# Kernel tuning notes

Hardware: AMD Instinct MI355X
Metric: run time of the kernel (lower is better)

The kernel has to match this reference:

```python
import jax, jax.numpy as jnp
import numpy as np

H, D = 8, 16
HID = H * D  # hidden_channels = 128
SQRT_D = float(np.sqrt(D))


def setup_inputs() -> dict:
    key = jax.random.key(0)
    ks = iter(jax.random.split(key, 64))
    def nrm(shape, scale):
        return jax.random.normal(next(ks), shape, dtype=jnp.float32) * scale
    def rint(n, hi):
        return jax.random.randint(next(ks), (n,), 0, hi, dtype=jnp.int32)
    E = 250000
    Nh, Ni, Nt = 8000, 40000, 20000
    inp = {
        'x_herb': nrm((Nh, 400), 1.0),
        'x_ing':  nrm((Ni, 300), 1.0),
        'x_tgt':  nrm((Nt, 200), 1.0),
        # per-type input projections
        'W_herb': nrm((400, HID), 0.05), 'b_herb': jnp.zeros((HID,), jnp.float32),
        'W_ing':  nrm((300, HID), 0.06), 'b_ing':  jnp.zeros((HID,), jnp.float32),
        'W_tgt':  nrm((200, HID), 0.07), 'b_tgt':  jnp.zeros((HID,), jnp.float32),
        # HGTConv per-node-type k/q/v linears, stacked over [herb, ing, tgt]
        'Wk': nrm((3, HID, HID), 0.09), 'bk': jnp.zeros((3, HID), jnp.float32),
        'Wq': nrm((3, HID, HID), 0.09), 'bq': jnp.zeros((3, HID), jnp.float32),
        'Wv': nrm((3, HID, HID), 0.09), 'bv': jnp.zeros((3, HID), jnp.float32),
        # per-edge-type relation matrices / priors, stacked over 4 edge types
        'a_rel': nrm((4, H, D, D), 0.25),
        'm_rel': nrm((4, H, D, D), 0.25),
        'p_rel': jnp.ones((4, H), jnp.float32),
        # per-dst-node-type output linear + skip gate
        'Wa': nrm((3, HID, HID), 0.09), 'ba': jnp.zeros((3, HID), jnp.float32),
        'skip': jnp.ones((3,), jnp.float32),
        # final herb linear
        'W_out': nrm((HID, HID), 0.09), 'b_out': jnp.zeros((HID,), jnp.float32),
        # edge lists: (herb->ing contains), (ing->herb rev), (ing->tgt targets), (tgt->ing rev)
        'src_ci': rint(E, Nh), 'dst_ci': rint(E, Ni),
        'src_ic': rint(E, Ni), 'dst_ic': rint(E, Nh),
        'src_it': rint(E, Ni), 'dst_it': rint(E, Nt),
        'src_ti': rint(E, Nt), 'dst_ti': rint(E, Ni),
    }
    return inp


def _hetero_forward(x_herb, x_ing, x_tgt, W_herb, b_herb, W_ing, b_ing, W_tgt, b_tgt,
                    Wk, bk, Wq, bq, Wv, bv, a_rel, m_rel, p_rel, Wa, ba, skip,
                    W_out, b_out, src_ci, dst_ci, src_ic, dst_ic, src_it, dst_it,
                    src_ti, dst_ti):
    types = ['herb', 'ing', 'tgt']
    xs = {'herb': x_herb @ W_herb + b_herb,
          'ing':  x_ing  @ W_ing  + b_ing,
          'tgt':  x_tgt  @ W_tgt  + b_tgt}
    Ns = {t: xs[t].shape[0] for t in types}
    # per-node-type k/q/v, reshaped to [N, H, D]
    k = {t: (xs[t] @ Wk[i] + bk[i]).reshape(-1, H, D) for i, t in enumerate(types)}
    q = {t: (xs[t] @ Wq[i] + bq[i]).reshape(-1, H, D) for i, t in enumerate(types)}
    v = {t: (xs[t] @ Wv[i] + bv[i]).reshape(-1, H, D) for i, t in enumerate(types)}

    edge_defs = [  # (edge_type_id, src_type, dst_type, src_idx, dst_idx)
        (0, 'herb', 'ing', src_ci, dst_ci),
        (1, 'ing', 'herb', src_ic, dst_ic),
        (2, 'ing', 'tgt', src_it, dst_it),
        (3, 'tgt', 'ing', src_ti, dst_ti),
    ]
    contrib = {t: [] for t in types}
    for e, s, t, src, dst in edge_defs:
        # relation-specific transforms at node level, then gather per edge
        k_rel = jnp.einsum('nhd,hde->nhe', k[s], a_rel[e])  # [Ns, H, D]
        v_rel = jnp.einsum('nhd,hde->nhe', v[s], m_rel[e])  # [Ns, H, D]
        logit = (q[t][dst] * k_rel[src]).sum(-1) * (p_rel[e] / SQRT_D)  # [E, H]
        contrib[t].append((logit, v_rel[src], dst))

    out = {}
    for i, t in enumerate(types):
        logits = jnp.concatenate([c[0] for c in contrib[t]], axis=0)  # [Et, H]
        msgs = jnp.concatenate([c[1] for c in contrib[t]], axis=0)    # [Et, H, D]
        dsts = jnp.concatenate([c[2] for c in contrib[t]], axis=0)    # [Et]
        n = Ns[t]
        # segment softmax over all incoming edges of each dst node (per head)
        mx = jax.ops.segment_max(logits, dsts, num_segments=n)
        ex = jnp.exp(logits - mx[dsts])
        den = jax.ops.segment_sum(ex, dsts, num_segments=n)
        alpha = ex / (den[dsts] + 1e-16)
        agg = jax.ops.segment_sum(msgs * alpha[:, :, None], dsts, num_segments=n)
        agg = agg.reshape(n, HID)
        o = jax.nn.gelu(agg, approximate=False) @ Wa[i] + ba[i]
        g = jax.nn.sigmoid(skip[i])
        out[t] = jax.nn.relu(g * o + (1.0 - g) * xs[t])
    out_herb = out['herb'] @ W_out + b_out
    return (out_herb, out['ing'], out['tgt'])


def reference(x_herb, x_ing, x_tgt, W_herb, b_herb, W_ing, b_ing, W_tgt, b_tgt,
              Wk, bk, Wq, bq, Wv, bv, a_rel, m_rel, p_rel, Wa, ba, skip,
              W_out, b_out, src_ci, dst_ci, src_ic, dst_ic, src_it, dst_it,
              src_ti, dst_ti):
    return _hetero_forward(x_herb, x_ing, x_tgt, W_herb, b_herb, W_ing, b_ing,
                           W_tgt, b_tgt, Wk, bk, Wq, bq, Wv, bv, a_rel, m_rel,
                           p_rel, Wa, ba, skip, W_out, b_out, src_ci, dst_ci,
                           src_ic, dst_ic, src_it, dst_it, src_ti, dst_ti)
```

## Files before the change

kernel.cpp:

```cpp
#include <hip/hip_runtime.h>
#include <math.h>

#define HID 128
typedef unsigned int uint;
typedef unsigned short ushort;
typedef __attribute__((ext_vector_type(8))) short short8;
typedef __attribute__((ext_vector_type(4))) float floatx4;
typedef __attribute__((ext_vector_type(2))) float f32x2;

__device__ __forceinline__ ushort f2b(float f) {
  uint u = __float_as_uint(f);
  u += 0x7fffu + ((u >> 16) & 1u);
  return (ushort)(u >> 16);
}
__device__ __forceinline__ float b2f(ushort s) {
  return __uint_as_float(((uint)s) << 16);
}
__device__ __forceinline__ float blo(uint u) { return __uint_as_float(u << 16); }
__device__ __forceinline__ float bhi(uint u) { return __uint_as_float(u & 0xffff0000u); }
__device__ __forceinline__ f32x2 b2x2(uint u) {
  f32x2 r;
  r.x = __uint_as_float(u << 16);
  r.y = __uint_as_float(u & 0xffff0000u);
  return r;
}

__device__ __forceinline__ void gll16(const ushort* g, ushort* l) {
  __builtin_amdgcn_global_load_lds(
      (const __attribute__((address_space(1))) void*)g,
      (__attribute__((address_space(3))) void*)l, 16, 0, 0);
}

__device__ __forceinline__ size_t a_packed_us(int rr, int col) {
  int tm = rr >> 7, prow = rr & 127;
  int ptk = col >> 5, kin = col & 31;
  int sw = (kin >> 3) ^ ((prow >> 1) & 3);
  return (((size_t)tm * 4 + ptk) * 512 + (size_t)prow * 4 + sw) * 8 + (kin & 7);
}

#define CSR_CH 2048
#define CSR_SH 9

struct EdgeStreams {
  const int* src[4]; const int* dst[4];
  int off[4]; uint rel[4]; uint ldb[4];
};

struct PackSeg { const float* X; ushort* out; int M, K, Ktiles, start; };
struct WBlk { const float* src; ushort* dst; int K; int start; };
struct Prolog {
  PackSeg pk[3];
  int crwstart, wstart, bstart, total;
  const float *Wk, *bk, *Wv, *bv, *a_rel, *m_rel, *p_rel;
  ushort* kw_dst[4];
  ushort* vw_dst[4];
  float* bcat;
  int kb_off[4], vb_off[4];
  WBlk wb[10];
  const float* bq;
  int bq_off[3];
  const int* edst[4];
  int eoff[4];
  uint* hist;
  int NBs, NBH, NBK, E;
};

__device__ void combine_rel_elem(const Prolog& P, int idx)
{
  int col  = idx & 127;
  int rest = idx >> 7;
  int row  = rest % 129;
  rest /= 129;
  int kv = rest & 1;
  int e  = rest >> 1;
  int i  = (e + 1) >> 1;
  int h = col >> 4, j = col & 15;
  const float* Wsrc = kv ? P.Wv : P.Wk;
  const float* bsrc = kv ? P.bv : P.bk;
  const float* rel  = kv ? P.m_rel : P.a_rel;
  float acc = 0.f;
  if (row < 128) {
#pragma unroll
    for (int d = 0; d < 16; ++d)
      acc += Wsrc[(size_t)i * 16384 + (size_t)row * 128 + h * 16 + d] *
             rel[((e * 8 + h) * 16 + d) * 16 + j];
  } else {
#pragma unroll
    for (int d = 0; d < 16; ++d)
      acc += bsrc[i * 128 + h * 16 + d] * rel[((e * 8 + h) * 16 + d) * 16 + j];
  }
  if (!kv) acc *= P.p_rel[e * 8 + h] * 0.36067376022224085f;
  if (row < 128) {
    ushort* dst = kv ? P.vw_dst[e] : P.kw_dst[e];
    int tk = row >> 5, chunk = (row >> 3) & 3, m = row & 7;
    int swf = chunk ^ ((col >> 1) & 3);
    dst[((tk * 512 + col * 4 + swf) << 3) + m] = f2b(acc);
  } else {
    P.bcat[(kv ? P.vb_off[e] : P.kb_off[e]) + col] = acc;
  }
}

__device__ void conv_elem(const Prolog& P, int s0)
{
  int si = 0;
#pragma unroll
  for (int k = 1; k < 10; ++k)
    if (s0 >= P.wb[k].start) si = k;
  WBlk b = P.wb[si];
  int s = s0 - b.start;
  int tk = s >> 9, o = s & 511;
  int c = o >> 2, swf = o & 3;
  int chunk = swf ^ ((c >> 1) & 3);
  int r0 = tk * 32 + chunk * 8;
  ushort tmp[8];
#pragma unroll
  for (int m = 0; m < 8; ++m) {
    int r = r0 + m;
    tmp[m] = (r < b.K) ? f2b(b.src[(size_t)r * 128 + c]) : (ushort)0;
  }
  *(short8*)&b.dst[(size_t)s * 8] = *(short8*)tmp;
}

__global__ __launch_bounds__(256)
void prologue(Prolog P)
{
  __shared__ uint h[512];
  int bI = blockIdx.x;
  if (bI < P.NBH) {
    int et = bI / P.NBs;
    int i0 = (bI - et * P.NBs) * CSR_CH;
    const int* dp = P.edst[et];
    int off = P.eoff[et];
    for (int t = threadIdx.x; t < P.NBK; t += 256) h[t] = 0;
    __syncthreads();
#pragma unroll
    for (int j = 0; j < CSR_CH / 256; ++j) {
      int idx = i0 + j * 256 + threadIdx.x;
      if (idx < P.E) atomicAdd(&h[(uint)(off + dp[idx]) >> CSR_SH], 1u);
    }
    __syncthreads();
    for (int t = threadIdx.x; t < P.NBK; t += 256)
      P.hist[(size_t)t * P.NBH + bI] = h[t];
    return;
  }
  int gtid = (bI - P.NBH) * 256 + threadIdx.x;
  if (gtid >= P.total) return;
  if (gtid >= P.bstart) {
    int j = gtid - P.bstart;
    P.bcat[P.bq_off[j >> 7] + (j & 127)] = P.bq[j];
    return;
  }
  if (gtid >= P.wstart) { conv_elem(P, gtid - P.wstart); return; }
  if (gtid >= P.crwstart) { combine_rel_elem(P, gtid - P.crwstart); return; }
  int si = 0;
  if (gtid >= P.pk[2].start) si = 2;
  else if (gtid >= P.pk[1].start) si = 1;
  const PackSeg s = P.pk[si];
  int slot = gtid - s.start;
  int spm = s.Ktiles << 9;
  int tm = slot / spm, r2 = slot - tm * spm;
  int tk = r2 >> 9, o = r2 & 511;
  int row = o >> 2, sw = o & 3;
  int chunk = sw ^ ((row >> 1) & 3);
  int grow = tm * 128 + row;
  int gk = tk * 32 + chunk * 8;
  ushort tmp[8];
  if (grow < s.M && gk + 8 <= s.K) {
    const float* p = s.X + (size_t)grow * s.K + gk;
    float4 a = *(const float4*)p, b = *(const float4*)(p + 4);
    tmp[0] = f2b(a.x); tmp[1] = f2b(a.y); tmp[2] = f2b(a.z); tmp[3] = f2b(a.w);
    tmp[4] = f2b(b.x); tmp[5] = f2b(b.y); tmp[6] = f2b(b.z); tmp[7] = f2b(b.w);
  } else {
#pragma unroll
    for (int j = 0; j < 8; ++j) {
      int kk = gk + j;
      tmp[j] = (grow < s.M && kk < s.K) ? f2b(s.X[(size_t)grow * s.K + kk]) : (ushort)0;
    }
  }
  *(short8*)&s.out[(size_t)slot * 8] = *(short8*)tmp;
}

__global__ __launch_bounds__(256)
void bucket_scan(uint* __restrict__ hist, uint* __restrict__ bucketTot, int NBH)
{
  __shared__ uint ws[4];
  __shared__ uint carry_s;
  int b = blockIdx.x;
  int t = threadIdx.x, lane = t & 63, w = t >> 6;
  if (t == 0) carry_s = 0;
  __syncthreads();
  for (int base = 0; base < NBH; base += 256) {
    int i = base + t;
    uint x = (i < NBH) ? hist[(size_t)b * NBH + i] : 0u;
    uint v = x;
#pragma unroll
    for (int o = 1; o < 64; o <<= 1) {
      uint y = __shfl_up(v, o, 64);
      if (lane >= o) v += y;
    }
    if (lane == 63) ws[w] = v;
    __syncthreads();
    uint add = carry_s;
    for (int k = 0; k < w; ++k) add += ws[k];
    if (i < NBH) hist[(size_t)b * NBH + i] = add + v - x;
    __syncthreads();
    if (t == 255) carry_s = add + v;
    __syncthreads();
  }
  if (t == 0) bucketTot[b] = carry_s;
}

__device__ __forceinline__ void base_scan(const uint* __restrict__ bucketTot,
                                          uint* sb, uint* ws, int NBK)
{
  int t = threadIdx.x, lane = t & 63, w = t >> 6;
  sb[t] = (t < NBK) ? bucketTot[t] : 0u;
  sb[t + 256] = (t + 256 < NBK) ? bucketTot[t + 256] : 0u;
  __syncthreads();
  uint a0 = sb[2 * t], a1 = sb[2 * t + 1];
  uint s = a0 + a1;
  uint v = s;
#pragma unroll
  for (int o = 1; o < 64; o <<= 1) {
    uint y = __shfl_up(v, o, 64);
    if (lane >= o) v += y;
  }
  if (lane == 63) ws[w] = v;
  __syncthreads();
  uint add = 0;
  for (int k = 0; k < w; ++k) add += ws[k];
  uint e0 = add + v - s;
  sb[2 * t] = e0;
  sb[2 * t + 1] = e0 + a0;
  __syncthreads();
}

__global__ __launch_bounds__(256)
void bucket_scatter(EdgeStreams es, const uint* __restrict__ hist,
                    const uint* __restrict__ bucketTot,
                    uint2* __restrict__ inter, int NBs, int NBH, int NBK, int E)
{
  __shared__ uint sb[516];
  __shared__ uint ws[4];
  __shared__ uint cur[512];
  base_scan(bucketTot, sb, ws, NBK);
  int b = blockIdx.x;
  int et = b / NBs;
  int i0 = (b - et * NBs) * CSR_CH;
  const int* dp = es.dst[et];
  const int* sp = es.src[et];
  int off = es.off[et];
  uint rel = es.rel[et], ldb = es.ldb[et];
  for (int t = threadIdx.x; t < NBK; t += 256)
    cur[t] = sb[t] + hist[(size_t)t * NBH + b];
  __syncthreads();
#pragma unroll
  for (int j = 0; j < CSR_CH / 256; ++j) {
    int idx = i0 + j * 256 + threadIdx.x;
    if (idx < E) {
      int g = off + dp[idx];
      uint pos = atomicAdd(&cur[(uint)g >> CSR_SH], 1u);
      inter[pos] = make_uint2(rel + (uint)sp[idx] * ldb, (uint)g);
    }
  }
}

__global__ __launch_bounds__(256)
void bucket_finalize(const uint2* __restrict__ inter,
                     const uint* __restrict__ bucketTot,
                     int* __restrict__ starts, uint* __restrict__ payload,
                     int Ntot, int NBK)
{
  __shared__ uint sb[516];
  __shared__ uint ncnt[512];
  __shared__ uint ws[4];
  base_scan(bucketTot, sb, ws, NBK);
  int b = blockIdx.x;
  int g0 = b << CSR_SH;
  int t = threadIdx.x, lane = t & 63, w = t >> 6;
  uint r0 = sb[b], r1 = sb[b + 1];
  if (b == NBK - 1 && t == 0) starts[Ntot] = (int)r1;
  ncnt[t] = 0; ncnt[t + 256] = 0;
  __syncthreads();
  for (uint i = r0 + t; i < r1; i += 256)
    atomicAdd(&ncnt[inter[i].y - g0], 1u);
  __syncthreads();
  uint a0 = ncnt[2 * t], a1 = ncnt[2 * t + 1];
  uint s = a0 + a1;
  uint v = s;
#pragma unroll
  for (int o = 1; o < 64; o <<= 1) {
    uint y = __shfl_up(v, o, 64);
    if (lane >= o) v += y;
  }
  if (lane == 63) ws[w] = v;
  __syncthreads();
  uint add = r0;
  for (int k = 0; k < w; ++k) add += ws[k];
  uint e0 = add + v - s;
  int gi = g0 + 2 * t;
  if (gi < Ntot)     starts[gi]     = (int)e0;
  if (gi + 1 < Ntot) starts[gi + 1] = (int)(e0 + a0);
  ncnt[2 * t] = e0;
  ncnt[2 * t + 1] = e0 + a0;
  __syncthreads();
  for (uint i = r0 + t; i < r1; i += 256) {
    uint2 rec = inter[i];
    uint pos = atomicAdd(&ncnt[rec.y - g0], 1u);
    payload[pos] = rec.x;
  }
}

struct GemmSeg {
  const ushort* A; const ushort* B; const float* bias;
  void* out; const ushort* xsP;
  int Ktiles, ldo, Mreal, skip_idx, epi, NT, start;
  int n2; const ushort* B2; const float* bias2;
  void* out2; int ldo2, Mreal2, epi2;
};
struct Gemm3 { GemmSeg s[3]; const float* skip; int nseg; };

__launch_bounds__(256)
__global__ void gemm_sched(Gemm3 g3)
{
  __shared__ __align__(16) ushort lds[20480];
  ushort* Xs = lds + 12288;

  int bid = blockIdx.x;
  int si = 0;
  if (g3.nseg > 1 && bid >= g3.s[1].start)
    si = (g3.nseg > 2 && bid >= g3.s[2].start) ? 2 : 1;
  const GemmSeg sg = g3.s[si];
  int local = bid - sg.start;
  int tmH = local / sg.NT, tn = local - tmH * sg.NT;
  int tm = tmH >> 1, hm = tmH & 1;

  const int t = threadIdx.x;
  const int wave = t >> 6, lane = t & 63;
  const int wn = wave * 32;
  const int l16 = lane & 15, quad = lane >> 4;
  const int Ktiles = sg.Ktiles;
  const int swz = (quad ^ ((l16 >> 1) & 3)) * 8;

  const ushort* Ahalf = sg.A + ((size_t)tm * Ktiles) * 4096 + hm * 2048;
  const ushort* Bbase = sg.B + (size_t)tn * Ktiles * 4096;

  floatx4 acc[4][2];
#pragma unroll
  for (int i = 0; i < 4; ++i)
#pragma unroll
    for (int j = 0; j < 2; ++j) acc[i][j] = (floatx4){0.f, 0.f, 0.f, 0.f};

  auto stage = [&](int tk, int buf) {
#pragma unroll
    for (int j = 0; j < 3; ++j) {
      int c = wave * 3 + j;
      if (c < 4)
        gll16(Ahalf + (size_t)tk * 4096 + c * 512 + lane * 8,
              lds + buf * 2048 + c * 512);
      else
        gll16(Bbase + (size_t)tk * 4096 + (c - 4) * 512 + lane * 8,
              lds + 4096 + buf * 4096 + (c - 4) * 512);
    }
  };
  auto stage2L = [&](int s2, int buf) {
#pragma unroll
    for (int j = 0; j < 2; ++j) {
      int c = wave * 2 + j;
      gll16(sg.B2 + (size_t)s2 * 4096 + c * 512 + lane * 8,
            lds + buf * 4096 + c * 512);
    }
  };

  stage(0, 0);
  __syncthreads();

  for (int tk = 0; tk < Ktiles; ++tk) {
    int buf = tk & 1;
    if (tk + 1 < Ktiles) stage(tk + 1, buf ^ 1);

    short8 af[4], bfr[2];
#pragma unroll
    for (int i = 0; i < 4; ++i)
      af[i] = *(const short8*)&lds[buf * 2048 + (i * 16 + l16) * 32 + swz];
#pragma unroll
    for (int n = 0; n < 2; ++n)
      bfr[n] = *(const short8*)&lds[4096 + buf * 4096 + (wn + n * 16 + l16) * 32 + swz];
#pragma unroll
    for (int mi = 0; mi < 4; ++mi)
#pragma unroll
      for (int ni = 0; ni < 2; ++ni)
        acc[mi][ni] = __builtin_amdgcn_mfma_f32_16x16x32_bf16(
            bfr[ni], af[mi], acc[mi][ni], 0, 0, 0);
    __syncthreads();
  }

  if (sg.n2 > 0) stage2L(0, 0);

  const int epi = sg.epi;
  float g = 0.f, omg = 0.f;
  if (epi == 2 || epi == 3 || epi == 5) {
    float s = g3.skip[sg.skip_idx];
    g = 1.f / (1.f + __expf(-s));
    omg = 1.f - g;
  }
#pragma unroll
  for (int ni = 0; ni < 2; ++ni) {
    int cl = wn + ni * 16 + quad * 4;
    int cb = tn * 128 + cl;
    float4 b4 = *(const float4*)&sg.bias[cb];
#pragma unroll
    for (int mi = 0; mi < 4; ++mi) {
      int prow = mi * 16 + l16;
      int rr = tm * 128 + hm * 64 + prow;
      float v0 = acc[mi][ni][0] + b4.x;
      float v1 = acc[mi][ni][1] + b4.y;
      float v2 = acc[mi][ni][2] + b4.z;
      float v3 = acc[mi][ni][3] + b4.w;
      if (epi == 0) {
        uint2 o = make_uint2(((uint)f2b(v1) << 16) | f2b(v0),
                             ((uint)f2b(v3) << 16) | f2b(v2));
        *(uint2*)&((ushort*)sg.out)[(size_t)rr * sg.ldo + cb] = o;
      } else if (epi == 1) {
        if (rr < sg.Mreal)
          *(float4*)&((float*)sg.out)[(size_t)rr * sg.ldo + cb] =
              make_float4(v0, v1, v2, v3);
      } else if (epi == 2) {
        if (rr < sg.Mreal) {
          uint2 xo = *(const uint2*)&sg.xsP[a_packed_us(rr, cb)];
          float4 o;
          o.x = fmaxf(g * v0 + omg * blo(xo.x), 0.f);
          o.y = fmaxf(g * v1 + omg * bhi(xo.x), 0.f);
          o.z = fmaxf(g * v2 + omg * blo(xo.y), 0.f);
          o.w = fmaxf(g * v3 + omg * bhi(xo.y), 0.f);
          *(float4*)&((float*)sg.out)[(size_t)rr * sg.ldo + cb] = o;
        }
      } else if (epi == 3) {
        uint2 xo = *(const uint2*)&sg.xsP[a_packed_us(rr, cb)];
        uint2 o = make_uint2(
            ((uint)f2b(fmaxf(g * v1 + omg * bhi(xo.x), 0.f)) << 16) |
                   f2b(fmaxf(g * v0 + omg * blo(xo.x), 0.f)),
            ((uint)f2b(fmaxf(g * v3 + omg * bhi(xo.y), 0.f)) << 16) |
                   f2b(fmaxf(g * v2 + omg * blo(xo.y), 0.f)));
        *(uint2*)&((ushort*)sg.out)[a_packed_us(rr, cb)] = o;
      } else if (epi == 4) {
        uint2 o = make_uint2(((uint)f2b(v1) << 16) | f2b(v0),
                             ((uint)f2b(v3) << 16) | f2b(v2));
        *(uint2*)&((ushort*)sg.out)[a_packed_us(rr, cb)] = o;
        int kin = cl & 31;
        int sw2 = (kin >> 3) ^ ((prow >> 1) & 3);
        *(uint2*)&Xs[(cl >> 5) * 2048 + prow * 32 + sw2 * 8 + (kin & 7)] = o;
      } else {
        uint2 xo = *(const uint2*)&sg.xsP[a_packed_us(rr, cb)];
        uint2 o = make_uint2(
            ((uint)f2b(fmaxf(g * v1 + omg * bhi(xo.x), 0.f)) << 16) |
                   f2b(fmaxf(g * v0 + omg * blo(xo.x), 0.f)),
            ((uint)f2b(fmaxf(g * v3 + omg * bhi(xo.y), 0.f)) << 16) |
                   f2b(fmaxf(g * v2 + omg * blo(xo.y), 0.f)));
        int kin = cl & 31;
        int sw2 = (kin >> 3) ^ ((prow >> 1) & 3);
        *(uint2*)&Xs[(cl >> 5) * 2048 + prow * 32 + sw2 * 8 + (kin & 7)] = o;
      }
    }
  }

  if (sg.n2 == 0) return;
  __syncthreads();
  int total2 = sg.n2 * 4;
  floatx4 a2[4][2];
#pragma unroll
  for (int i = 0; i < 4; ++i)
#pragma unroll
    for (int j = 0; j < 2; ++j) a2[i][j] = (floatx4){0.f, 0.f, 0.f, 0.f};
  for (int s2 = 0; s2 < total2; ++s2) {
    int buf = s2 & 1;
    if (s2 + 1 < total2) stage2L(s2 + 1, buf ^ 1);
    int xb = (s2 & 3) * 2048;
    short8 af[4], bfr[2];
#pragma unroll
    for (int i = 0; i < 4; ++i)
      af[i] = *(const short8*)&Xs[xb + (i * 16 + l16) * 32 + swz];
#pragma unroll
    for (int n = 0; n < 2; ++n)
      bfr[n] = *(const short8*)&lds[buf * 4096 + (wn + n * 16 + l16) * 32 + swz];
#pragma unroll
    for (int mi = 0; mi < 4; ++mi)
#pragma unroll
      for (int ni = 0; ni < 2; ++ni)
        a2[mi][ni] = __builtin_amdgcn_mfma_f32_16x16x32_bf16(
            bfr[ni], af[mi], a2[mi][ni], 0, 0, 0);
    __syncthreads();
    if ((s2 & 3) == 3) {
      int t2 = s2 >> 2;
#pragma unroll
      for (int ni = 0; ni < 2; ++ni) {
        int cb2 = t2 * 128 + wn + ni * 16 + quad * 4;
        float4 b4 = *(const float4*)&sg.bias2[cb2];
#pragma unroll
        for (int mi = 0; mi < 4; ++mi) {
          int rr = tm * 128 + hm * 64 + mi * 16 + l16;
          float v0 = a2[mi][ni][0] + b4.x;
          float v1 = a2[mi][ni][1] + b4.y;
          float v2 = a2[mi][ni][2] + b4.z;
          float v3 = a2[mi][ni][3] + b4.w;
          if (sg.epi2 == 0) {
            uint2 o = make_uint2(((uint)f2b(v1) << 16) | f2b(v0),
                                 ((uint)f2b(v3) << 16) | f2b(v2));
            *(uint2*)&((ushort*)sg.out2)[(size_t)rr * sg.ldo2 + cb2] = o;
          } else {
            if (rr < sg.Mreal2)
              *(float4*)&((float*)sg.out2)[(size_t)rr * sg.ldo2 + cb2] =
                  make_float4(v0, v1, v2, v3);
          }
          a2[mi][ni] = (floatx4){0.f, 0.f, 0.f, 0.f};
        }
      }
    }
  }
}

struct GatherType { const ushort* q; ushort* agg; int ldq; };
struct GatherDesc { GatherType ty[3]; int n0, n1; };

__launch_bounds__(256)
__global__ void gather_all(const int* __restrict__ starts,
                           const uint* __restrict__ payload,
                           const ushort* __restrict__ kvbase,
                           GatherDesc gd, int Ntot)
{
  int wid = (blockIdx.x * 256 + threadIdx.x) >> 6;
  if (wid >= Ntot) return;
  int lane = threadIdx.x & 63;
  int g = lane >> 4, l = lane & 15;

  GatherType T;
  int d;
  if (wid < gd.n0)      { T = gd.ty[0]; d = wid; }
  else if (wid < gd.n1) { T = gd.ty[1]; d = wid - gd.n0; }
  else                  { T = gd.ty[2]; d = wid - gd.n1; }

  const char* kvb = (const char*)kvbase;
  const uint lofs = (uint)l * 16u;

  uint4 qv = *(const uint4*)(T.q + (size_t)d * T.ldq + l * 8);
  f32x2 q0 = b2x2(qv.x), q1 = b2x2(qv.y), q2 = b2x2(qv.z), q3 = b2x2(qv.w);

  int e0 = starts[wid], e1 = starts[wid + 1];
  float lsum = 0.f;
  f32x2 ac0 = {0.f, 0.f}, ac1 = {0.f, 0.f}, ac2 = {0.f, 0.f}, ac3 = {0.f, 0.f};

  for (int eb = e0; eb < e1; eb += 8) {
    int eA = eb + g, eB = eA + 4;
    bool actA = eA < e1, actB = eB < e1;
    uint pA = payload[actA ? eA : e0];
    uint pB = payload[actB ? eB : e0];
    const char* bA = kvb + (pA + lofs);
    const char* bB = kvb + (pB + lofs);
    uint4 kA = *(const uint4*)bA;
    uint4 vA = *(const uint4*)(bA + 256);
    uint4 kB = *(const uint4*)bB;
    uint4 vB = *(const uint4*)(bB + 256);

    f32x2 dA = q0 * b2x2(kA.x);
    dA = __builtin_elementwise_fma(q1, b2x2(kA.y), dA);
    dA = __builtin_elementwise_fma(q2, b2x2(kA.z), dA);
    dA = __builtin_elementwise_fma(q3, b2x2(kA.w), dA);
    f32x2 dB = q0 * b2x2(kB.x);
    dB = __builtin_elementwise_fma(q1, b2x2(kB.y), dB);
    dB = __builtin_elementwise_fma(q2, b2x2(kB.z), dB);
    dB = __builtin_elementwise_fma(q3, b2x2(kB.w), dB);
    float pa = dA.x + dA.y;
    float pb = dB.x + dB.y;
    pa += __shfl_xor(pa, 1, 64);
    pb += __shfl_xor(pb, 1, 64);
    float exA = exp2f(fminf(pa, 115.4f));
    float exB = exp2f(fminf(pb, 115.4f));
    exA = actA ? exA : 0.f;
    exB = actB ? exB : 0.f;
    lsum += exA + exB;
    f32x2 xA = {exA, exA}, xB = {exB, exB};
    ac0 = __builtin_elementwise_fma(xA, b2x2(vA.x), ac0);
    ac1 = __builtin_elementwise_fma(xA, b2x2(vA.y), ac1);
    ac2 = __builtin_elementwise_fma(xA, b2x2(vA.z), ac2);
    ac3 = __builtin_elementwise_fma(xA, b2x2(vA.w), ac3);
    ac0 = __builtin_elementwise_fma(xB, b2x2(vB.x), ac0);
    ac1 = __builtin_elementwise_fma(xB, b2x2(vB.y), ac1);
    ac2 = __builtin_elementwise_fma(xB, b2x2(vB.z), ac2);
    ac3 = __builtin_elementwise_fma(xB, b2x2(vB.w), ac3);
  }

  float s0 = ac0.x, s1 = ac0.y, s2 = ac1.x, s3 = ac1.y;
  float s4 = ac2.x, s5 = ac2.y, s6 = ac3.x, s7 = ac3.y;
#define MRG(v) v += __shfl_xor(v, 16, 64); v += __shfl_xor(v, 32, 64)
  MRG(lsum); MRG(s0); MRG(s1); MRG(s2); MRG(s3); MRG(s4); MRG(s5); MRG(s6); MRG(s7);
#undef MRG

  float inv = 1.f / (lsum + 1e-16f);
  float m0 = (g & 1) ? s2 : s0, m1 = (g & 1) ? s6 : s4;
  float n0 = (g & 1) ? s3 : s1, n1 = (g & 1) ? s7 : s5;
  float x0 = ((g & 2) ? m1 : m0) * inv;
  float x1 = ((g & 2) ? n1 : n0) * inv;
  float g0 = 0.5f * x0 * (1.f + erff(x0 * 0.70710678118654752f));
  float g1 = 0.5f * x1 * (1.f + erff(x1 * 0.70710678118654752f));
  int tm = d >> 7, row = d & 127;
  int tk = l >> 2, sw = (l & 3) ^ ((row >> 1) & 3);
  size_t us = (((size_t)tm * 4 + tk) * 512 + (size_t)row * 4 + sw) * 8 + 2 * g;
  *(uint*)(T.agg + us) = ((uint)f2b(g1) << 16) | (uint)f2b(g0);
}

extern "C" void kernel_launch(void* const* d_in, const int* in_sizes, int n_in,
                              void* d_out, int out_size, void* d_ws, size_t ws_size,
                              hipStream_t stream)
{
  const float* x_herb = (const float*)d_in[0];
  const float* x_ing  = (const float*)d_in[1];
  const float* x_tgt  = (const float*)d_in[2];
  const float* W_herb = (const float*)d_in[3];
  const float* b_herb = (const float*)d_in[4];
  const float* W_ing  = (const float*)d_in[5];
  const float* b_ing  = (const float*)d_in[6];
  const float* W_tgt  = (const float*)d_in[7];
  const float* b_tgt  = (const float*)d_in[8];
  const float* Wk     = (const float*)d_in[9];
  const float* bk     = (const float*)d_in[10];
  const float* Wq     = (const float*)d_in[11];
  const float* bq     = (const float*)d_in[12];
  const float* Wv     = (const float*)d_in[13];
  const float* bv     = (const float*)d_in[14];
  const float* a_rel  = (const float*)d_in[15];
  const float* m_rel  = (const float*)d_in[16];
  const float* p_rel  = (const float*)d_in[17];
  const float* Wa     = (const float*)d_in[18];
  const float* ba     = (const float*)d_in[19];
  const float* skip   = (const float*)d_in[20];
  const float* W_out  = (const float*)d_in[21];
  const float* b_out  = (const float*)d_in[22];
  const int* srcs[4] = {(const int*)d_in[23], (const int*)d_in[25],
                        (const int*)d_in[27], (const int*)d_in[29]};
  const int* dsts[4] = {(const int*)d_in[24], (const int*)d_in[26],
                        (const int*)d_in[28], (const int*)d_in[30]};

  const int Nh = in_sizes[0] / 400;
  const int Ni = in_sizes[1] / 300;
  const int Nt = in_sizes[2] / 200;
  const int E  = in_sizes[23];
  const int Ntot = Nh + Ni + Nt;

  const int MT_h = (Nh + 127) / 128, MT_i = (Ni + 127) / 128, MT_t = (Nt + 127) / 128;
  const int KT_h = 13, KT_i = 10, KT_t = 7;

  const int NBs = (E + CSR_CH - 1) / CSR_CH;
  const int NBH = 4 * NBs;
  const int NBK = (Ntot + (1 << CSR_SH) - 1) >> CSR_SH;

  char* base = (char*)d_ws;
  size_t off = 0;
  auto A = [&](size_t bytes) -> void* {
    void* p = base + off; off += (bytes + 255) & ~(size_t)255; return p;
  };
  ushort* xp_h  = (ushort*)A((size_t)MT_h * KT_h * 8192);
  ushort* xp_i  = (ushort*)A((size_t)MT_i * KT_i * 8192);
  ushort* xp_t  = (ushort*)A((size_t)MT_t * KT_t * 8192);
  ushort* xsP_h = (ushort*)A((size_t)MT_h * 4 * 8192);
  ushort* xsP_i = (ushort*)A((size_t)MT_i * 4 * 8192);
  ushort* xsP_t = (ushort*)A((size_t)MT_t * 4 * 8192);
  ushort* fused_h = (ushort*)A((size_t)MT_h * 128 * 384 * 2);
  ushort* fused_i = (ushort*)A((size_t)MT_i * 128 * 640 * 2);
  ushort* fused_t = (ushort*)A((size_t)MT_t * 128 * 384 * 2);
  ushort* aggp_h  = (ushort*)A((size_t)MT_h * 4 * 8192);
  ushort* aggp_i  = (ushort*)A((size_t)MT_i * 4 * 8192);
  ushort* aggp_t  = (ushort*)A((size_t)MT_t * 4 * 8192);
  ushort* Weff1_h = (ushort*)A((size_t)KT_h * 8192);
  ushort* Weff1_i = (ushort*)A((size_t)KT_i * 8192);
  ushort* Weff1_t = (ushort*)A((size_t)KT_t * 8192);
  ushort* Wcat_h = (ushort*)A((size_t)3 * 4 * 8192);
  ushort* Wcat_i = (ushort*)A((size_t)5 * 4 * 8192);
  ushort* Wcat_t = (ushort*)A((size_t)3 * 4 * 8192);
  float* bcat   = (float*)A(1408 * 4);
  ushort* Wa_t   = (ushort*)A((size_t)3 * 16384 * 2);
  ushort* Wout_t = (ushort*)A((size_t)16384 * 2);
  int* starts  = (int*)A((size_t)(Ntot + 4) * 4);
  uint* payload = (uint*)A((size_t)(4 * E + 8) * 4);
  uint* hist    = (uint*)A((size_t)NBK * NBH * 4);
  uint* bucketTot  = (uint*)A((size_t)NBK * 4);
  uint2* inter  = (uint2*)A((size_t)(4 * E + 8) * 8);
  (void)ws_size; (void)n_in;

  const int toff_h = 0, toff_i = Nh, toff_t = Nh + Ni;
  dim3 blk(256);

  uint fi2 = (uint)((size_t)(fused_i - fused_h) * 2);
  uint ft2 = (uint)((size_t)(fused_t - fused_h) * 2);

  int sl_h = MT_h * KT_h * 512, sl_i = MT_i * KT_i * 512, sl_t = MT_t * KT_t * 512;
  Prolog P;
  P.pk[0] = {x_herb, xp_h, Nh, 400, KT_h, 0};
  P.pk[1] = {x_ing,  xp_i, Ni, 300, KT_i, sl_h};
  P.pk[2] = {x_tgt,  xp_t, Nt, 200, KT_t, sl_h + sl_i};
  P.crwstart = sl_h + sl_i + sl_t;
  P.wstart = P.crwstart + 4 * 2 * 129 * 128;
  {
    const float* wsrc10[10] = {W_herb, W_ing, W_tgt, Wq, Wq + 16384, Wq + 32768,
                               Wa, Wa + 16384, Wa + 32768, W_out};
    ushort* wdst10[10] = {Weff1_h, Weff1_i, Weff1_t, Wcat_h, Wcat_i, Wcat_t,
                          Wa_t, Wa_t + 16384, Wa_t + 32768, Wout_t};
    int wk10[10] = {400, 300, 200, 128, 128, 128, 128, 128, 128, 128};
    int wcum = 0;
    for (int z = 0; z < 10; ++z) {
      P.wb[z] = {wsrc10[z], wdst10[z], wk10[z], wcum};
      wcum += ((wk10[z] + 31) / 32) * 512;
    }
    P.bstart = P.wstart + wcum;
  }
  P.total = P.bstart + 384;
  P.Wk = Wk; P.bk = bk; P.Wv = Wv; P.bv = bv;
  P.a_rel = a_rel; P.m_rel = m_rel; P.p_rel = p_rel;
  P.kw_dst[0] = Wcat_h + 16384; P.vw_dst[0] = Wcat_h + 32768;
  P.kw_dst[1] = Wcat_i + 16384; P.vw_dst[1] = Wcat_i + 32768;
  P.kw_dst[2] = Wcat_i + 49152; P.vw_dst[2] = Wcat_i + 65536;
  P.kw_dst[3] = Wcat_t + 16384; P.vw_dst[3] = Wcat_t + 32768;
  P.bcat = bcat;
  P.kb_off[0] = 128;  P.vb_off[0] = 256;
  P.kb_off[1] = 512;  P.vb_off[1] = 640;
  P.kb_off[2] = 768;  P.vb_off[2] = 896;
  P.kb_off[3] = 1152; P.vb_off[3] = 1280;
  P.bq = bq;
  P.bq_off[0] = 0; P.bq_off[1] = 384; P.bq_off[2] = 1024;
  P.edst[0] = dsts[0]; P.eoff[0] = toff_i;
  P.edst[1] = dsts[1]; P.eoff[1] = toff_h;
  P.edst[2] = dsts[2]; P.eoff[2] = toff_t;
  P.edst[3] = dsts[3]; P.eoff[3] = toff_i;
  P.hist = hist; P.NBs = NBs; P.NBH = NBH; P.NBK = NBK; P.E = E;
  prologue<<<NBH + (P.total + 255) / 256, blk, 0, stream>>>(P);

  EdgeStreams ES;
  ES.src[0] = srcs[0]; ES.dst[0] = dsts[0]; ES.off[0] = toff_i;
  ES.rel[0] = 256u;        ES.ldb[0] = 768u;
  ES.src[1] = srcs[1]; ES.dst[1] = dsts[1]; ES.off[1] = toff_h;
  ES.rel[1] = fi2 + 256u;  ES.ldb[1] = 1280u;
  ES.src[2] = srcs[2]; ES.dst[2] = dsts[2]; ES.off[2] = toff_t;
  ES.rel[2] = fi2 + 768u;  ES.ldb[2] = 1280u;
  ES.src[3] = srcs[3]; ES.dst[3] = dsts[3]; ES.off[3] = toff_i;
  ES.rel[3] = ft2 + 256u;  ES.ldb[3] = 768u;
  bucket_scan<<<NBK, blk, 0, stream>>>(hist, bucketTot, NBH);
  bucket_scatter<<<NBH, blk, 0, stream>>>(ES, hist, bucketTot, inter, NBs, NBH, NBK, E);
  bucket_finalize<<<NBK, blk, 0, stream>>>(inter, bucketTot, starts, payload, Ntot, NBK);

  Gemm3 G1;
  G1.skip = skip; G1.nseg = 3;
  G1.s[0] = {xp_h, Weff1_h, b_herb, xsP_h, nullptr, KT_h, 0, 0, 0, 4, 1, 0,
             3, Wcat_h, bcat + 0, fused_h, 384, 0, 0};
  G1.s[1] = {xp_i, Weff1_i, b_ing,  xsP_i, nullptr, KT_i, 0, 0, 0, 4, 1, 2 * MT_h,
             5, Wcat_i, bcat + 384, fused_i, 640, 0, 0};
  G1.s[2] = {xp_t, Weff1_t, b_tgt,  xsP_t, nullptr, KT_t, 0, 0, 0, 4, 1,
             2 * (MT_h + MT_i),
             3, Wcat_t, bcat + 1024, fused_t, 384, 0, 0};
  gemm_sched<<<2 * (MT_h + MT_i + MT_t), blk, 0, stream>>>(G1);

  GatherDesc GD;
  GD.n0 = Nh; GD.n1 = Nh + Ni;
  GD.ty[0] = {fused_h, aggp_h, 384};
  GD.ty[1] = {fused_i, aggp_i, 640};
  GD.ty[2] = {fused_t, aggp_t, 384};
  gather_all<<<(Ntot + 3) / 4, blk, 0, stream>>>(starts, payload, fused_h, GD, Ntot);

  float* outp = (float*)d_out;
  float* out_herb = outp;
  float* out_ing  = outp + (size_t)Nh * HID;
  float* out_tgt  = outp + (size_t)(Nh + Ni) * HID;
  Gemm3 GE;
  GE.skip = skip; GE.nseg = 3;
  GE.s[0] = {aggp_h, Wa_t + 0 * 16384, ba + 0 * 128, nullptr, xsP_h,
             4, 0, 0, 0, 5, 1, 0,
             1, Wout_t, b_out, out_herb, 128, Nh, 1};
  GE.s[1] = {aggp_i, Wa_t + 1 * 16384, ba + 1 * 128, out_ing, xsP_i,
             4, 128, Ni, 1, 2, 1, 2 * MT_h,
             0, nullptr, nullptr, nullptr, 0, 0, 0};
  GE.s[2] = {aggp_t, Wa_t + 2 * 16384, ba + 2 * 128, out_tgt, xsP_t,
             4, 128, Nt, 2, 2, 1, 2 * (MT_h + MT_i),
             0, nullptr, nullptr, nullptr, 0, 0, 0};
  gemm_sched<<<2 * (MT_h + MT_i + MT_t), blk, 0, stream>>>(GE);
  (void)out_size;
}
```

Measured before the change: 378.9 us.

## Fuse fp32-to-bf16 input packing into first GEMM A-tile staging

Removes the prologue stage that converted x_herb/x_ing/x_tgt to swizzled bf16 tiles in a global scratch buffer. The first GEMM now loads fp32 rows directly, converts them to bf16 in registers and writes them into the swizzled LDS layout. The B operand keeps its async global-to-LDS load. This drops one full write and read of the packed inputs and shrinks the prologue, at the cost of synchronous fp32 loads and conversions in the GEMM's staging path, which may reduce overlap with the MFMA work.

```diff
diff --git a/kernel.cpp b/kernel.cpp
--- a/kernel.cpp
+++ b/kernel.cpp
@@ -46,11 +46,9 @@
   int off[4]; uint rel[4]; uint ldb[4];
 };
 
-struct PackSeg { const float* X; ushort* out; int M, K, Ktiles, start; };
 struct WBlk { const float* src; ushort* dst; int K; int start; };
 struct Prolog {
-  PackSeg pk[3];
-  int crwstart, wstart, bstart, total;
+  int wstart, bstart, total;
   const float *Wk, *bk, *Wv, *bv, *a_rel, *m_rel, *p_rel;
   ushort* kw_dst[4];
   ushort* vw_dst[4];
@@ -151,33 +149,7 @@
     return;
   }
   if (gtid >= P.wstart) { conv_elem(P, gtid - P.wstart); return; }
-  if (gtid >= P.crwstart) { combine_rel_elem(P, gtid - P.crwstart); return; }
-  int si = 0;
-  if (gtid >= P.pk[2].start) si = 2;
-  else if (gtid >= P.pk[1].start) si = 1;
-  const PackSeg s = P.pk[si];
-  int slot = gtid - s.start;
-  int spm = s.Ktiles << 9;
-  int tm = slot / spm, r2 = slot - tm * spm;
-  int tk = r2 >> 9, o = r2 & 511;
-  int row = o >> 2, sw = o & 3;
-  int chunk = sw ^ ((row >> 1) & 3);
-  int grow = tm * 128 + row;
-  int gk = tk * 32 + chunk * 8;
-  ushort tmp[8];
-  if (grow < s.M && gk + 8 <= s.K) {
-    const float* p = s.X + (size_t)grow * s.K + gk;
-    float4 a = *(const float4*)p, b = *(const float4*)(p + 4);
-    tmp[0] = f2b(a.x); tmp[1] = f2b(a.y); tmp[2] = f2b(a.z); tmp[3] = f2b(a.w);
-    tmp[4] = f2b(b.x); tmp[5] = f2b(b.y); tmp[6] = f2b(b.z); tmp[7] = f2b(b.w);
-  } else {
-#pragma unroll
-    for (int j = 0; j < 8; ++j) {
-      int kk = gk + j;
-      tmp[j] = (grow < s.M && kk < s.K) ? f2b(s.X[(size_t)grow * s.K + kk]) : (ushort)0;
-    }
-  }
-  *(short8*)&s.out[(size_t)slot * 8] = *(short8*)tmp;
+  combine_rel_elem(P, gtid);
 }
 
 __global__ __launch_bounds__(256)
@@ -317,6 +289,7 @@
   int Ktiles, ldo, Mreal, skip_idx, epi, NT, start;
   int n2; const ushort* B2; const float* bias2;
   void* out2; int ldo2, Mreal2, epi2;
+  const float* Af; int Kf, Mf;
 };
 struct Gemm3 { GemmSeg s[3]; const float* skip; int nseg; };
 
@@ -345,22 +318,46 @@
   const ushort* Ahalf = sg.A + ((size_t)tm * Ktiles) * 4096 + hm * 2048;
   const ushort* Bbase = sg.B + (size_t)tn * Ktiles * 4096;
 
+  const int aprow = t >> 2, asw = t & 3;
+  const int achunk = asw ^ ((aprow >> 1) & 3);
+  const int agrow = tm * 128 + hm * 64 + aprow;
+  const bool arowok = (sg.Af == nullptr) || (agrow < sg.Mf);
+  const float* axrow = sg.Af + (size_t)(arowok ? agrow : 0) * sg.Kf;
+
   floatx4 acc[4][2];
 #pragma unroll
   for (int i = 0; i < 4; ++i)
 #pragma unroll
     for (int j = 0; j < 2; ++j) acc[i][j] = (floatx4){0.f, 0.f, 0.f, 0.f};
 
-  auto stage = [&](int tk, int buf) {
-#pragma unroll
-    for (int j = 0; j < 3; ++j) {
-      int c = wave * 3 + j;
-      if (c < 4)
-        gll16(Ahalf + (size_t)tk * 4096 + c * 512 + lane * 8,
-              lds + buf * 2048 + c * 512);
-      else
-        gll16(Bbase + (size_t)tk * 4096 + (c - 4) * 512 + lane * 8,
-              lds + 4096 + buf * 4096 + (c - 4) * 512);
+  auto stageA = [&](int tk, int buf) {
+    if (sg.Af == nullptr) {
+      gll16(Ahalf + (size_t)tk * 4096 + wave * 512 + lane * 8,
+            lds + buf * 2048 + wave * 512);
+    } else {
+      int gk = tk * 32 + achunk * 8;
+      ushort tmp[8];
+      if (arowok && gk + 8 <= sg.Kf) {
+        const float* p = axrow + gk;
+        float4 a = *(const float4*)p, b = *(const float4*)(p + 4);
+        tmp[0] = f2b(a.x); tmp[1] = f2b(a.y); tmp[2] = f2b(a.z); tmp[3] = f2b(a.w);
+        tmp[4] = f2b(b.x); tmp[5] = f2b(b.y); tmp[6] = f2b(b.z); tmp[7] = f2b(b.w);
+      } else {
+#pragma unroll
+        for (int j = 0; j < 8; ++j) {
+          int kk = gk + j;
+          tmp[j] = (arowok && kk < sg.Kf) ? f2b(axrow[kk]) : (ushort)0;
+        }
+      }
+      *(short8*)&lds[buf * 2048 + t * 8] = *(short8*)tmp;
+    }
+  };
+  auto stageB = [&](int tk, int buf) {
+#pragma unroll
+    for (int j = 0; j < 2; ++j) {
+      int c = wave * 2 + j;
+      gll16(Bbase + (size_t)tk * 4096 + c * 512 + lane * 8,
+            lds + 4096 + buf * 4096 + c * 512);
     }
   };
   auto stage2L = [&](int s2, int buf) {
@@ -372,12 +369,13 @@
     }
   };
 
-  stage(0, 0);
+  stageB(0, 0);
+  stageA(0, 0);
   __syncthreads();
 
   for (int tk = 0; tk < Ktiles; ++tk) {
     int buf = tk & 1;
-    if (tk + 1 < Ktiles) stage(tk + 1, buf ^ 1);
+    if (tk + 1 < Ktiles) { stageB(tk + 1, buf ^ 1); stageA(tk + 1, buf ^ 1); }
 
     short8 af[4], bfr[2];
 #pragma unroll
@@ -658,9 +656,6 @@
   auto A = [&](size_t bytes) -> void* {
     void* p = base + off; off += (bytes + 255) & ~(size_t)255; return p;
   };
-  ushort* xp_h  = (ushort*)A((size_t)MT_h * KT_h * 8192);
-  ushort* xp_i  = (ushort*)A((size_t)MT_i * KT_i * 8192);
-  ushort* xp_t  = (ushort*)A((size_t)MT_t * KT_t * 8192);
   ushort* xsP_h = (ushort*)A((size_t)MT_h * 4 * 8192);
   ushort* xsP_i = (ushort*)A((size_t)MT_i * 4 * 8192);
   ushort* xsP_t = (ushort*)A((size_t)MT_t * 4 * 8192);
@@ -692,13 +687,8 @@
   uint fi2 = (uint)((size_t)(fused_i - fused_h) * 2);
   uint ft2 = (uint)((size_t)(fused_t - fused_h) * 2);
 
-  int sl_h = MT_h * KT_h * 512, sl_i = MT_i * KT_i * 512, sl_t = MT_t * KT_t * 512;
   Prolog P;
-  P.pk[0] = {x_herb, xp_h, Nh, 400, KT_h, 0};
-  P.pk[1] = {x_ing,  xp_i, Ni, 300, KT_i, sl_h};
-  P.pk[2] = {x_tgt,  xp_t, Nt, 200, KT_t, sl_h + sl_i};
-  P.crwstart = sl_h + sl_i + sl_t;
-  P.wstart = P.crwstart + 4 * 2 * 129 * 128;
+  P.wstart = 4 * 2 * 129 * 128;
   {
     const float* wsrc10[10] = {W_herb, W_ing, W_tgt, Wq, Wq + 16384, Wq + 32768,
                                Wa, Wa + 16384, Wa + 32768, W_out};
@@ -748,13 +738,13 @@
 
   Gemm3 G1;
   G1.skip = skip; G1.nseg = 3;
-  G1.s[0] = {xp_h, Weff1_h, b_herb, xsP_h, nullptr, KT_h, 0, 0, 0, 4, 1, 0,
-             3, Wcat_h, bcat + 0, fused_h, 384, 0, 0};
-  G1.s[1] = {xp_i, Weff1_i, b_ing,  xsP_i, nullptr, KT_i, 0, 0, 0, 4, 1, 2 * MT_h,
-             5, Wcat_i, bcat + 384, fused_i, 640, 0, 0};
-  G1.s[2] = {xp_t, Weff1_t, b_tgt,  xsP_t, nullptr, KT_t, 0, 0, 0, 4, 1,
+  G1.s[0] = {nullptr, Weff1_h, b_herb, xsP_h, nullptr, KT_h, 0, 0, 0, 4, 1, 0,
+             3, Wcat_h, bcat + 0, fused_h, 384, 0, 0, x_herb, 400, Nh};
+  G1.s[1] = {nullptr, Weff1_i, b_ing,  xsP_i, nullptr, KT_i, 0, 0, 0, 4, 1, 2 * MT_h,
+             5, Wcat_i, bcat + 384, fused_i, 640, 0, 0, x_ing, 300, Ni};
+  G1.s[2] = {nullptr, Weff1_t, b_tgt,  xsP_t, nullptr, KT_t, 0, 0, 0, 4, 1,
              2 * (MT_h + MT_i),
-             3, Wcat_t, bcat + 1024, fused_t, 384, 0, 0};
+             3, Wcat_t, bcat + 1024, fused_t, 384, 0, 0, x_tgt, 200, Nt};
   gemm_sched<<<2 * (MT_h + MT_i + MT_t), blk, 0, stream>>>(G1);
 
   GatherDesc GD;
@@ -772,13 +762,13 @@
   GE.skip = skip; GE.nseg = 3;
   GE.s[0] = {aggp_h, Wa_t + 0 * 16384, ba + 0 * 128, nullptr, xsP_h,
              4, 0, 0, 0, 5, 1, 0,
-             1, Wout_t, b_out, out_herb, 128, Nh, 1};
+             1, Wout_t, b_out, out_herb, 128, Nh, 1, nullptr, 0, 0};
   GE.s[1] = {aggp_i, Wa_t + 1 * 16384, ba + 1 * 128, out_ing, xsP_i,
              4, 128, Ni, 1, 2, 1, 2 * MT_h,
-             0, nullptr, nullptr, nullptr, 0, 0, 0};
+             0, nullptr, nullptr, nullptr, 0, 0, 0, nullptr, 0, 0};
   GE.s[2] = {aggp_t, Wa_t + 2 * 16384, ba + 2 * 128, out_tgt, xsP_t,
              4, 128, Nt, 2, 2, 1, 2 * (MT_h + MT_i),
-             0, nullptr, nullptr, nullptr, 0, 0, 0};
+             0, nullptr, nullptr, nullptr, 0, 0, 0, nullptr, 0, 0};
   gemm_sched<<<2 * (MT_h + MT_i + MT_t), blk, 0, stream>>>(GE);
   (void)out_size;
 }
```

New measurement: 367.3 us. 1.03x faster.
